# Kernel optimization log

Measured on AMD Instinct MI355X. Metric: run time of the kernel, lower is better.

The kernel has to match this reference:

```python
import jax, jax.numpy as jnp
from jax import lax
import numpy as np

B, CIN, H, W = 8, 3, 512, 512
BASE = 32
TOPK = 200
SCORE_T = 0.01
IOU_T = 0.5
DN = ('NCHW', 'OIHW', 'NCHW')


def setup_inputs() -> dict:
    key = jax.random.key(0)
    ks = jax.random.split(key, 12)
    def conv_w(k, o, i, kh, kw):
        fan_in = i * kh * kw
        return jax.random.normal(k, (o, i, kh, kw), jnp.float32) * (1.0 / np.sqrt(fan_in))
    c = [CIN, BASE, BASE * 2, BASE * 4, BASE * 8]
    inp = {'images': jax.random.normal(ks[0], (B, CIN, H, W), jnp.float32)}
    for l in range(4):
        inp[f'w{l+1}'] = conv_w(ks[1 + 2 * l], c[l + 1], c[l], 3, 3)
        inp[f'b{l+1}'] = jnp.zeros((c[l + 1],), jnp.float32)
    inp['wh'] = conv_w(ks[9], 5, c[4], 1, 1)
    inp['bh'] = jnp.zeros((5,), jnp.float32)
    return inp


def _conv_relu_pool(x, w, b):
    x = lax.conv_general_dilated(x, w, (1, 1), 'SAME', dimension_numbers=DN)
    x = jax.nn.relu(x + b[None, :, None, None])
    return lax.reduce_window(x, -jnp.inf, lax.max, (1, 1, 2, 2), (1, 1, 2, 2), 'VALID')


def _decode(pred):
    # pred: [B,5,Gh,Gw]
    Bn, _, Gh, Gw = pred.shape
    sy, sx = H / float(Gh), W / float(Gw)
    obj = jax.nn.sigmoid(pred[:, 0])
    tx = jax.nn.sigmoid(pred[:, 1])
    ty = jax.nn.sigmoid(pred[:, 2])
    bw = jnp.exp(pred[:, 3]) * sx
    bh = jnp.exp(pred[:, 4]) * sy
    gy = jnp.arange(Gh, dtype=pred.dtype)[None, :, None]
    gx = jnp.arange(Gw, dtype=pred.dtype)[None, None, :]
    cx = gx * sx + tx * sx
    cy = gy * sy + ty * sy
    x1 = jnp.clip(cx - bw / 2.0, 0.0, W - 1)
    y1 = jnp.clip(cy - bh / 2.0, 0.0, H - 1)
    x2 = jnp.clip(cx + bw / 2.0, 0.0, W - 1)
    y2 = jnp.clip(cy + bh / 2.0, 0.0, H - 1)
    boxes = jnp.stack([x1, y1, x2, y2], axis=-1).reshape(Bn, Gh * Gw, 4)
    scores = obj.reshape(Bn, Gh * Gw)
    # score threshold + top-k (fixed size, padded with invalid entries)
    masked = jnp.where(scores >= SCORE_T, scores, -1.0)
    svals, sidx = lax.top_k(masked, TOPK)                      # [B,K]
    boxes_k = jnp.take_along_axis(boxes, sidx[:, :, None], axis=1)  # [B,K,4]
    valid = svals >= SCORE_T
    # pairwise IoU [B,K,K]
    bx1, by1, bx2, by2 = (boxes_k[..., i] for i in range(4))
    area = (bx2 - bx1) * (by2 - by1)
    xx1 = jnp.maximum(bx1[:, :, None], bx1[:, None, :])
    yy1 = jnp.maximum(by1[:, :, None], by1[:, None, :])
    xx2 = jnp.minimum(bx2[:, :, None], bx2[:, None, :])
    yy2 = jnp.minimum(by2[:, :, None], by2[:, None, :])
    inter = jnp.clip(xx2 - xx1, 0.0) * jnp.clip(yy2 - yy1, 0.0)
    union = area[:, :, None] + area[:, None, :] - inter
    iou = inter / jnp.maximum(union, 1e-6)
    ar = jnp.arange(TOPK)
    def body(i, keep):  # greedy NMS over score-sorted boxes
        sup = (iou[:, i, :] > IOU_T) & (ar[None, :] > i) & keep[:, i][:, None]
        return keep & ~sup
    keep = lax.fori_loop(0, TOPK, body, valid)
    scores_k = jnp.where(valid, svals, 0.0)
    return boxes_k, scores_k, keep


def reference(images, w1, b1, w2, b2, w3, b3, w4, b4, wh, bh):
    x = _conv_relu_pool(images, w1, b1)
    x = _conv_relu_pool(x, w2, b2)
    x = _conv_relu_pool(x, w3, b3)
    x = _conv_relu_pool(x, w4, b4)
    pred = lax.conv_general_dilated(x, wh, (1, 1), 'SAME', dimension_numbers=DN)
    pred = pred + bh[None, :, None, None]
    boxes, scores, keep = _decode(pred)
    kf = keep.astype(boxes.dtype)
    out5 = jnp.concatenate([boxes, scores[..., None]], axis=-1) * kf[..., None]
    return out5, keep
```

## Files before the change

### kernel.cpp

```cpp
#include <hip/hip_runtime.h>
#include <math.h>


constexpr int TOPK_N = 200;

template <int CIN, int CI_BLK, int CO_BLK>
__launch_bounds__(256)
__global__ void conv_relu_pool_tiled(const float* __restrict__ in,
                                     const float* __restrict__ wgt,
                                     const float* __restrict__ bias,
                                     float* __restrict__ out,
                                     int Hin, int Win, int Cout) {
    constexpr int SPATIAL = 34 * 34;
    constexpr int SSLOT = (SPATIAL + 255) / 256;
    const int Hp = Hin >> 1, Wp = Win >> 1;
    const int coChunks = Cout / CO_BLK;
    const int b  = blockIdx.z / coChunks;
    const int cz = blockIdx.z % coChunks;
    const int tid = threadIdx.x;
    const int tx = tid & 15, ty = tid >> 4;
    const int px = (blockIdx.x << 4) + tx;
    const int py = (blockIdx.y << 4) + ty;
    const int iy0 = (blockIdx.y << 5) - 1;
    const int ix0 = (blockIdx.x << 5) - 1;

    __shared__ float  s_in[CI_BLK][34][34];
    __shared__ double s_w[CI_BLK * 9 * CO_BLK];
    float* s_in_flat = &s_in[0][0][0];

    int soff[SSLOT];
#pragma unroll
    for (int s = 0; s < SSLOT; ++s) {
        const int cell = tid + s * 256;
        int g = -1;
        if (cell < SPATIAL) {
            const int ly = cell / 34, lx = cell - ly * 34;
            const int iy = iy0 + ly, ix = ix0 + lx;
            if ((unsigned)iy < (unsigned)Hin && (unsigned)ix < (unsigned)Win)
                g = iy * Win + ix;
        }
        soff[s] = g;
    }
    const size_t HW = (size_t)Hin * Win;
    const float* in_b = in + (size_t)b * CIN * HW;

    double acc[CO_BLK][4];
#pragma unroll
    for (int co = 0; co < CO_BLK; ++co)
#pragma unroll
        for (int p = 0; p < 4; ++p) acc[co][p] = 0.0;

    for (int c0 = 0; c0 < CIN; c0 += CI_BLK) {
#pragma unroll
        for (int ci = 0; ci < CI_BLK; ++ci) {
            const float* src = in_b + (c0 + ci) * HW;
#pragma unroll
            for (int s = 0; s < SSLOT; ++s) {
                const int cell = tid + s * 256;
                if (cell < SPATIAL) {
                    const int g = soff[s];
                    float v = 0.f;
                    if (g >= 0) v = src[g];
                    s_in_flat[ci * SPATIAL + cell] = v;
                }
            }
        }
        for (int idx = tid; idx < CI_BLK * 9 * CO_BLK; idx += 256) {
            int co   = idx & (CO_BLK - 1);
            int rest = idx / CO_BLK;
            int k    = rest % 9;
            int ci   = rest / 9;
            s_w[idx] = (double)wgt[((cz * CO_BLK + co) * CIN + c0 + ci) * 9 + k];
        }
        __syncthreads();

#pragma unroll 1
        for (int ci = 0; ci < CI_BLK; ++ci) {
            double win[4][4];
#pragma unroll
            for (int iy = 0; iy < 4; ++iy) {
                float2 r0 = *(const float2*)&s_in[ci][2 * ty + iy][2 * tx];
                float2 r1 = *(const float2*)&s_in[ci][2 * ty + iy][2 * tx + 2];
                win[iy][0] = (double)r0.x; win[iy][1] = (double)r0.y;
                win[iy][2] = (double)r1.x; win[iy][3] = (double)r1.y;
            }
#pragma unroll
            for (int k = 0; k < 9; ++k) {
                const int ky = k / 3, kx = k % 3;
                const double* wp = &s_w[(ci * 9 + k) * CO_BLK];
                double w[CO_BLK];
#pragma unroll
                for (int co = 0; co < CO_BLK; ++co) w[co] = wp[co];
#pragma unroll
                for (int p = 0; p < 4; ++p) {
                    const double v = win[(p >> 1) + ky][(p & 1) + kx];
#pragma unroll
                    for (int co = 0; co < CO_BLK; ++co)
                        acc[co][p] = fma(v, w[co], acc[co][p]);
                }
            }
        }
        __syncthreads();
    }

#pragma unroll
    for (int co = 0; co < CO_BLK; ++co) {
        const double bd = (double)bias[cz * CO_BLK + co];
        const float e0 = fmaxf((float)(acc[co][0] + bd), 0.f);
        const float e1 = fmaxf((float)(acc[co][1] + bd), 0.f);
        const float e2 = fmaxf((float)(acc[co][2] + bd), 0.f);
        const float e3 = fmaxf((float)(acc[co][3] + bd), 0.f);
        out[((size_t)(b * Cout + cz * CO_BLK + co) * Hp + py) * Wp + px] =
            fmaxf(fmaxf(e0, e1), fmaxf(e2, e3));
    }
}

__launch_bounds__(256)
__global__ void head_decode_k(const float* __restrict__ x4,
                              const float* __restrict__ wh,
                              const float* __restrict__ bh,
                              float* __restrict__ boxes,
                              float* __restrict__ scores) {
    __shared__ float s_wh[5 * 256];
    const int tid = threadIdx.x;
#pragma unroll
    for (int i = 0; i < 5; ++i) s_wh[i * 256 + tid] = wh[i * 256 + tid];
    __syncthreads();

    const int idx  = blockIdx.x * 256 + tid;
    const int b    = idx >> 10;
    const int cell = idx & 1023;
    const int gy = cell >> 5, gx = cell & 31;

    double a0 = (double)bh[0], a1 = (double)bh[1], a2 = (double)bh[2],
           a3 = (double)bh[3], a4 = (double)bh[4];
    const float* xp = x4 + b * 262144 + cell;
    for (int ci = 0; ci < 256; ++ci) {
        const double v = (double)xp[ci << 10];
        a0 = fma(v, (double)s_wh[0 * 256 + ci], a0);
        a1 = fma(v, (double)s_wh[1 * 256 + ci], a1);
        a2 = fma(v, (double)s_wh[2 * 256 + ci], a2);
        a3 = fma(v, (double)s_wh[3 * 256 + ci], a3);
        a4 = fma(v, (double)s_wh[4 * 256 + ci], a4);
    }
    const double obj = 1.0 / (1.0 + exp(-a0));
    const double txs = 1.0 / (1.0 + exp(-a1));
    const double tys = 1.0 / (1.0 + exp(-a2));
    const double bw  = exp(a3) * 16.0;
    const double bhh = exp(a4) * 16.0;
    const double cx  = gx * 16.0 + txs * 16.0;
    const double cy  = gy * 16.0 + tys * 16.0;
    float* bp = boxes + idx * 4;
    bp[0] = (float)fmin(fmax(cx - bw * 0.5, 0.0), 511.0);
    bp[1] = (float)fmin(fmax(cy - bhh * 0.5, 0.0), 511.0);
    bp[2] = (float)fmin(fmax(cx + bw * 0.5, 0.0), 511.0);
    bp[3] = (float)fmin(fmax(cy + bhh * 0.5, 0.0), 511.0);
    scores[idx] = (float)obj;
}

__launch_bounds__(256)
__global__ void topk_nms_k(const float* __restrict__ boxes,
                           const float* __restrict__ scores,
                           float* __restrict__ out5,
                           float* __restrict__ keep_out) {
    const int b = blockIdx.x, tid = threadIdx.x;
    __shared__ unsigned long long key[1024];
    __shared__ float bx1[TOPK_N], by1[TOPK_N], bx2[TOPK_N], by2[TOPK_N];
    __shared__ float sv[TOPK_N], ar[TOPK_N];
    __shared__ int   kp[TOPK_N];

    for (int i = tid; i < 1024; i += 256) {
        float s = scores[b * 1024 + i];
        float m = (s >= 0.01f) ? s : -1.0f;
        unsigned u = __float_as_uint(m);
        u = (u & 0x80000000u) ? ~u : (u | 0x80000000u);
        key[i] = ((unsigned long long)u << 32) | (unsigned)(1023 - i);
    }
    __syncthreads();

    for (int k = 2; k <= 1024; k <<= 1) {
        for (int j = k >> 1; j > 0; j >>= 1) {
            for (int i = tid; i < 1024; i += 256) {
                int l = i ^ j;
                if (l > i) {
                    unsigned long long a = key[i], c = key[l];
                    bool desc = ((i & k) == 0);
                    bool sw = desc ? (a < c) : (a > c);
                    if (sw) { key[i] = c; key[l] = a; }
                }
            }
            __syncthreads();
        }
    }

    for (int i = tid; i < TOPK_N; i += 256) {
        unsigned long long kk = key[i];
        unsigned u = (unsigned)(kk >> 32);
        unsigned bits = (u & 0x80000000u) ? (u & 0x7FFFFFFFu) : ~u;
        float s = __uint_as_float(bits);
        int src = 1023 - (int)(kk & 0xFFFFFFFFu);
        const float4 bb = *(const float4*)(boxes + (b * 1024 + src) * 4);
        bx1[i] = bb.x; by1[i] = bb.y; bx2[i] = bb.z; by2[i] = bb.w;
        sv[i] = s;
        ar[i] = (bb.z - bb.x) * (bb.w - bb.y);
        kp[i] = (s >= 0.01f) ? 1 : 0;
    }
    __syncthreads();

    for (int i = 0; i < TOPK_N; ++i) {
        if (kp[i]) {
            const float X1 = bx1[i], Y1 = by1[i], X2 = bx2[i], Y2 = by2[i], A = ar[i];
            for (int j = tid; j < TOPK_N; j += 256) {
                if (j > i && kp[j]) {
                    float xx1 = fmaxf(X1, bx1[j]);
                    float yy1 = fmaxf(Y1, by1[j]);
                    float xx2 = fminf(X2, bx2[j]);
                    float yy2 = fminf(Y2, by2[j]);
                    float inter = fmaxf(xx2 - xx1, 0.f) * fmaxf(yy2 - yy1, 0.f);
                    float uni = A + ar[j] - inter;
                    float iou = inter / fmaxf(uni, 1e-6f);
                    if (iou > 0.5f) kp[j] = 0;
                }
            }
        }
        __syncthreads();
    }

    for (int i = tid; i < TOPK_N; i += 256) {
        float kf = kp[i] ? 1.f : 0.f;
        float s  = sv[i];
        float sc = (s >= 0.01f) ? s : 0.f;
        float* op = out5 + (b * TOPK_N + i) * 5;
        op[0] = bx1[i] * kf;
        op[1] = by1[i] * kf;
        op[2] = bx2[i] * kf;
        op[3] = by2[i] * kf;
        op[4] = sc * kf;
        keep_out[b * TOPK_N + i] = kf;
    }
}

extern "C" void kernel_launch(void* const* d_in, const int* in_sizes, int n_in,
                              void* d_out, int out_size, void* d_ws, size_t ws_size,
                              hipStream_t stream) {
    const float* images = (const float*)d_in[0];
    const float* w1 = (const float*)d_in[1];
    const float* b1 = (const float*)d_in[2];
    const float* w2 = (const float*)d_in[3];
    const float* b2 = (const float*)d_in[4];
    const float* w3 = (const float*)d_in[5];
    const float* b3 = (const float*)d_in[6];
    const float* w4 = (const float*)d_in[7];
    const float* b4 = (const float*)d_in[8];
    const float* wh = (const float*)d_in[9];
    const float* bh = (const float*)d_in[10];
    float* out = (float*)d_out;

    float* A    = (float*)d_ws;
    float* Bbuf = A + 16777216;
    float* boxes  = A + 8388608;
    float* scores = A + 8388608 + 32768;

    conv_relu_pool_tiled<3, 3, 8><<<dim3(16, 16, 8 * 4), 256, 0, stream>>>(
        images, w1, b1, A, 512, 512, 32);
    conv_relu_pool_tiled<32, 2, 8><<<dim3(8, 8, 8 * 8), 256, 0, stream>>>(
        A, w2, b2, Bbuf, 256, 256, 64);
    conv_relu_pool_tiled<64, 2, 8><<<dim3(4, 4, 8 * 16), 256, 0, stream>>>(
        Bbuf, w3, b3, A, 128, 128, 128);
    conv_relu_pool_tiled<128, 2, 8><<<dim3(2, 2, 8 * 32), 256, 0, stream>>>(
        A, w4, b4, Bbuf, 64, 64, 256);
    head_decode_k<<<32, 256, 0, stream>>>(Bbuf, wh, bh, boxes, scores);
    topk_nms_k<<<8, 256, 0, stream>>>(boxes, scores, out, out + 8 * TOPK_N * 5);
}
```

Before: 1.500 ms.

## Double-buffer input and weight tiles in conv-relu-pool kernels via register prefetch

The conv-relu-pool kernel now keeps two shared-memory buffers for the input halo tile and the weights. While the current channel chunk is being computed, the loads for the next chunk are issued into registers, then written to the other buffer with a single barrier per chunk. The goal is to hide global-load latency behind the fp64 FMA work and to remove one of the two barriers per iteration. In exchange it doubles shared-memory use and adds register pressure from the prefetch registers, which may lower occupancy. The weight prefetch assumes NW is at most 256 (one weight per thread), which holds for the current configurations.

Measured after the change: 1.341 ms. 10.6% less time.

```diff
diff --git a/kernel.cpp b/kernel.cpp
--- a/kernel.cpp
+++ b/kernel.cpp
@@ -6,13 +6,15 @@
 
 template <int CIN, int CI_BLK, int CO_BLK>
 __launch_bounds__(256)
-__global__ void conv_relu_pool_tiled(const float* __restrict__ in,
-                                     const float* __restrict__ wgt,
-                                     const float* __restrict__ bias,
-                                     float* __restrict__ out,
-                                     int Hin, int Win, int Cout) {
+__global__ void conv_relu_pool_pipe(const float* __restrict__ in,
+                                    const float* __restrict__ wgt,
+                                    const float* __restrict__ bias,
+                                    float* __restrict__ out,
+                                    int Hin, int Win, int Cout) {
     constexpr int SPATIAL = 34 * 34;
     constexpr int SSLOT = (SPATIAL + 255) / 256;
+    constexpr int NW = CI_BLK * 9 * CO_BLK;
+    constexpr int NCHUNK = CIN / CI_BLK;
     const int Hp = Hin >> 1, Wp = Win >> 1;
     const int coChunks = Cout / CO_BLK;
     const int b  = blockIdx.z / coChunks;
@@ -24,9 +26,8 @@
     const int iy0 = (blockIdx.y << 5) - 1;
     const int ix0 = (blockIdx.x << 5) - 1;
 
-    __shared__ float  s_in[CI_BLK][34][34];
-    __shared__ double s_w[CI_BLK * 9 * CO_BLK];
-    float* s_in_flat = &s_in[0][0][0];
+    __shared__ float  s_in[2][CI_BLK * SPATIAL];
+    __shared__ double s_w[2][NW];
 
     int soff[SSLOT];
 #pragma unroll
@@ -41,6 +42,14 @@
         }
         soff[s] = g;
     }
+    int wg = -1;
+    if (tid < NW) {
+        const int co   = tid & (CO_BLK - 1);
+        const int rest = tid / CO_BLK;
+        const int k    = rest % 9;
+        const int ci   = rest / 9;
+        wg = ((cz * CO_BLK + co) * CIN + ci) * 9 + k;
+    }
     const size_t HW = (size_t)Hin * Win;
     const float* in_b = in + (size_t)b * CIN * HW;
 
@@ -50,44 +59,63 @@
 #pragma unroll
         for (int p = 0; p < 4; ++p) acc[co][p] = 0.0;
 
-    for (int c0 = 0; c0 < CIN; c0 += CI_BLK) {
-#pragma unroll
-        for (int ci = 0; ci < CI_BLK; ++ci) {
-            const float* src = in_b + (c0 + ci) * HW;
-#pragma unroll
-            for (int s = 0; s < SSLOT; ++s) {
-                const int cell = tid + s * 256;
-                if (cell < SPATIAL) {
-                    const int g = soff[s];
+    float rin[CI_BLK][SSLOT];
+    float rw = 0.f;
+
+#pragma unroll
+    for (int ci = 0; ci < CI_BLK; ++ci) {
+        const float* src = in_b + ci * HW;
+#pragma unroll
+        for (int s = 0; s < SSLOT; ++s) {
+            const int cell = tid + s * 256;
+            float v = 0.f;
+            if (cell < SPATIAL) { const int g = soff[s]; if (g >= 0) v = src[g]; }
+            rin[ci][s] = v;
+        }
+    }
+    if (tid < NW) rw = wgt[wg];
+#pragma unroll
+    for (int ci = 0; ci < CI_BLK; ++ci)
+#pragma unroll
+        for (int s = 0; s < SSLOT; ++s) {
+            const int cell = tid + s * 256;
+            if (cell < SPATIAL) s_in[0][ci * SPATIAL + cell] = rin[ci][s];
+        }
+    if (tid < NW) s_w[0][tid] = (double)rw;
+    __syncthreads();
+
+    for (int c = 0; c < NCHUNK; ++c) {
+        const int buf = c & 1;
+        if (c + 1 < NCHUNK) {
+            const int c0n = (c + 1) * CI_BLK;
+#pragma unroll
+            for (int ci = 0; ci < CI_BLK; ++ci) {
+                const float* src = in_b + (c0n + ci) * HW;
+#pragma unroll
+                for (int s = 0; s < SSLOT; ++s) {
+                    const int cell = tid + s * 256;
                     float v = 0.f;
-                    if (g >= 0) v = src[g];
-                    s_in_flat[ci * SPATIAL + cell] = v;
-                }
-            }
-        }
-        for (int idx = tid; idx < CI_BLK * 9 * CO_BLK; idx += 256) {
-            int co   = idx & (CO_BLK - 1);
-            int rest = idx / CO_BLK;
-            int k    = rest % 9;
-            int ci   = rest / 9;
-            s_w[idx] = (double)wgt[((cz * CO_BLK + co) * CIN + c0 + ci) * 9 + k];
-        }
-        __syncthreads();
-
+                    if (cell < SPATIAL) { const int g = soff[s]; if (g >= 0) v = src[g]; }
+                    rin[ci][s] = v;
+                }
+            }
+            if (tid < NW) rw = wgt[wg + c0n * 9];
+        }
 #pragma unroll 1
         for (int ci = 0; ci < CI_BLK; ++ci) {
+            const float* tile = &s_in[buf][ci * SPATIAL];
             double win[4][4];
 #pragma unroll
             for (int iy = 0; iy < 4; ++iy) {
-                float2 r0 = *(const float2*)&s_in[ci][2 * ty + iy][2 * tx];
-                float2 r1 = *(const float2*)&s_in[ci][2 * ty + iy][2 * tx + 2];
+                float2 r0 = *(const float2*)&tile[(2 * ty + iy) * 34 + 2 * tx];
+                float2 r1 = *(const float2*)&tile[(2 * ty + iy) * 34 + 2 * tx + 2];
                 win[iy][0] = (double)r0.x; win[iy][1] = (double)r0.y;
                 win[iy][2] = (double)r1.x; win[iy][3] = (double)r1.y;
             }
 #pragma unroll
             for (int k = 0; k < 9; ++k) {
                 const int ky = k / 3, kx = k % 3;
-                const double* wp = &s_w[(ci * 9 + k) * CO_BLK];
+                const double* wp = &s_w[buf][(ci * 9 + k) * CO_BLK];
                 double w[CO_BLK];
 #pragma unroll
                 for (int co = 0; co < CO_BLK; ++co) w[co] = wp[co];
@@ -100,7 +128,17 @@
                 }
             }
         }
-        __syncthreads();
+        if (c + 1 < NCHUNK) {
+#pragma unroll
+            for (int ci = 0; ci < CI_BLK; ++ci)
+#pragma unroll
+                for (int s = 0; s < SSLOT; ++s) {
+                    const int cell = tid + s * 256;
+                    if (cell < SPATIAL) s_in[buf ^ 1][ci * SPATIAL + cell] = rin[ci][s];
+                }
+            if (tid < NW) s_w[buf ^ 1][tid] = (double)rw;
+            __syncthreads();
+        }
     }
 
 #pragma unroll
@@ -261,13 +299,13 @@
     float* boxes  = A + 8388608;
     float* scores = A + 8388608 + 32768;
 
-    conv_relu_pool_tiled<3, 3, 8><<<dim3(16, 16, 8 * 4), 256, 0, stream>>>(
+    conv_relu_pool_pipe<3, 3, 8><<<dim3(16, 16, 8 * 4), 256, 0, stream>>>(
         images, w1, b1, A, 512, 512, 32);
-    conv_relu_pool_tiled<32, 2, 8><<<dim3(8, 8, 8 * 8), 256, 0, stream>>>(
+    conv_relu_pool_pipe<32, 2, 8><<<dim3(8, 8, 8 * 8), 256, 0, stream>>>(
         A, w2, b2, Bbuf, 256, 256, 64);
-    conv_relu_pool_tiled<64, 2, 8><<<dim3(4, 4, 8 * 16), 256, 0, stream>>>(
+    conv_relu_pool_pipe<64, 2, 8><<<dim3(4, 4, 8 * 16), 256, 0, stream>>>(
         Bbuf, w3, b3, A, 128, 128, 128);
-    conv_relu_pool_tiled<128, 2, 8><<<dim3(2, 2, 8 * 32), 256, 0, stream>>>(
+    conv_relu_pool_pipe<128, 2, 8><<<dim3(2, 2, 8 * 32), 256, 0, stream>>>(
         A, w4, b4, Bbuf, 64, 64, 256);
     head_decode_k<<<32, 256, 0, stream>>>(Bbuf, wh, bh, boxes, scores);
     topk_nms_k<<<8, 256, 0, stream>>>(boxes, scores, out, out + 8 * TOPK_N * 5);
```

## Load conv input windows directly from global memory with register prefetch

Applied to the files above, without the earlier changes.

Drops the shared-memory input tile in the conv+relu+pool kernel. Each thread now loads its own 4x4 input window straight from global memory into registers and prefetches the next channel's window while computing the current one. Weights are still staged in shared memory, now in larger channel chunks so fewer barriers are needed. The cost is redundant global loads, since neighbouring threads re-read overlapping pixels, plus extra register pressure, in exchange for removing the tile staging and its synchronisation.

New measurement: 1.516 ms. About the same (+1.1%).

```diff
diff --git a/kernel.cpp b/kernel.cpp
--- a/kernel.cpp
+++ b/kernel.cpp
@@ -4,15 +4,14 @@
 
 constexpr int TOPK_N = 200;
 
-template <int CIN, int CI_BLK, int CO_BLK>
+template <int CIN, int CI_CHUNK, int CO_BLK>
 __launch_bounds__(256)
-__global__ void conv_relu_pool_tiled(const float* __restrict__ in,
-                                     const float* __restrict__ wgt,
-                                     const float* __restrict__ bias,
-                                     float* __restrict__ out,
-                                     int Hin, int Win, int Cout) {
-    constexpr int SPATIAL = 34 * 34;
-    constexpr int SSLOT = (SPATIAL + 255) / 256;
+__global__ void conv_direct(const float* __restrict__ in,
+                            const float* __restrict__ wgt,
+                            const float* __restrict__ bias,
+                            float* __restrict__ out,
+                            int Hin, int Win, int Cout) {
+    constexpr int NW = CI_CHUNK * 9 * CO_BLK;
     const int Hp = Hin >> 1, Wp = Win >> 1;
     const int coChunks = Cout / CO_BLK;
     const int b  = blockIdx.z / coChunks;
@@ -21,25 +20,21 @@
     const int tx = tid & 15, ty = tid >> 4;
     const int px = (blockIdx.x << 4) + tx;
     const int py = (blockIdx.y << 4) + ty;
-    const int iy0 = (blockIdx.y << 5) - 1;
-    const int ix0 = (blockIdx.x << 5) - 1;
-
-    __shared__ float  s_in[CI_BLK][34][34];
-    __shared__ double s_w[CI_BLK * 9 * CO_BLK];
-    float* s_in_flat = &s_in[0][0][0];
-
-    int soff[SSLOT];
-#pragma unroll
-    for (int s = 0; s < SSLOT; ++s) {
-        const int cell = tid + s * 256;
-        int g = -1;
-        if (cell < SPATIAL) {
-            const int ly = cell / 34, lx = cell - ly * 34;
-            const int iy = iy0 + ly, ix = ix0 + lx;
-            if ((unsigned)iy < (unsigned)Hin && (unsigned)ix < (unsigned)Win)
-                g = iy * Win + ix;
-        }
-        soff[s] = g;
+    const int y0 = 2 * py, x0 = 2 * px;
+
+    __shared__ double s_w[NW];
+
+    int rowE[4], colE[4];
+    float rowM[4], colM[4];
+#pragma unroll
+    for (int d = 0; d < 4; ++d) {
+        int iy = y0 - 1 + d;
+        rowM[d] = (iy >= 0 && iy < Hin) ? 1.f : 0.f;
+        iy = min(max(iy, 0), Hin - 1);
+        rowE[d] = iy * Win;
+        int ix = x0 - 1 + d;
+        colM[d] = (ix >= 0 && ix < Win) ? 1.f : 0.f;
+        colE[d] = min(max(ix, 0), Win - 1);
     }
     const size_t HW = (size_t)Hin * Win;
     const float* in_b = in + (size_t)b * CIN * HW;
@@ -50,44 +45,48 @@
 #pragma unroll
         for (int p = 0; p < 4; ++p) acc[co][p] = 0.0;
 
-    for (int c0 = 0; c0 < CIN; c0 += CI_BLK) {
-#pragma unroll
-        for (int ci = 0; ci < CI_BLK; ++ci) {
-            const float* src = in_b + (c0 + ci) * HW;
-#pragma unroll
-            for (int s = 0; s < SSLOT; ++s) {
-                const int cell = tid + s * 256;
-                if (cell < SPATIAL) {
-                    const int g = soff[s];
-                    float v = 0.f;
-                    if (g >= 0) v = src[g];
-                    s_in_flat[ci * SPATIAL + cell] = v;
-                }
-            }
-        }
-        for (int idx = tid; idx < CI_BLK * 9 * CO_BLK; idx += 256) {
-            int co   = idx & (CO_BLK - 1);
-            int rest = idx / CO_BLK;
-            int k    = rest % 9;
-            int ci   = rest / 9;
-            s_w[idx] = (double)wgt[((cz * CO_BLK + co) * CIN + c0 + ci) * 9 + k];
-        }
+    float raw[16];
+    {
+        const float* src = in_b;
+#pragma unroll
+        for (int dy = 0; dy < 4; ++dy)
+#pragma unroll
+            for (int dx = 0; dx < 4; ++dx)
+                raw[dy * 4 + dx] = src[rowE[dy] + colE[dx]];
+    }
+
+    for (int c0 = 0; c0 < CIN; c0 += CI_CHUNK) {
         __syncthreads();
+        for (int idx = tid; idx < NW; idx += 256) {
+            const int co   = idx & (CO_BLK - 1);
+            const int rest = idx / CO_BLK;
+            const int k    = rest % 9;
+            const int ciL  = rest / 9;
+            s_w[idx] = (double)wgt[((cz * CO_BLK + co) * CIN + c0 + ciL) * 9 + k];
+        }
+        __syncthreads();
 
 #pragma unroll 1
-        for (int ci = 0; ci < CI_BLK; ++ci) {
+        for (int ciL = 0; ciL < CI_CHUNK; ++ciL) {
+            const int ci = c0 + ciL;
             double win[4][4];
 #pragma unroll
-            for (int iy = 0; iy < 4; ++iy) {
-                float2 r0 = *(const float2*)&s_in[ci][2 * ty + iy][2 * tx];
-                float2 r1 = *(const float2*)&s_in[ci][2 * ty + iy][2 * tx + 2];
-                win[iy][0] = (double)r0.x; win[iy][1] = (double)r0.y;
-                win[iy][2] = (double)r1.x; win[iy][3] = (double)r1.y;
+            for (int dy = 0; dy < 4; ++dy)
+#pragma unroll
+                for (int dx = 0; dx < 4; ++dx)
+                    win[dy][dx] = (double)(raw[dy * 4 + dx] * rowM[dy] * colM[dx]);
+            if (ci + 1 < CIN) {
+                const float* src = in_b + (size_t)(ci + 1) * HW;
+#pragma unroll
+                for (int dy = 0; dy < 4; ++dy)
+#pragma unroll
+                    for (int dx = 0; dx < 4; ++dx)
+                        raw[dy * 4 + dx] = src[rowE[dy] + colE[dx]];
             }
 #pragma unroll
             for (int k = 0; k < 9; ++k) {
                 const int ky = k / 3, kx = k % 3;
-                const double* wp = &s_w[(ci * 9 + k) * CO_BLK];
+                const double* wp = &s_w[(ciL * 9 + k) * CO_BLK];
                 double w[CO_BLK];
 #pragma unroll
                 for (int co = 0; co < CO_BLK; ++co) w[co] = wp[co];
@@ -100,7 +99,6 @@
                 }
             }
         }
-        __syncthreads();
     }
 
 #pragma unroll
@@ -261,13 +259,13 @@
     float* boxes  = A + 8388608;
     float* scores = A + 8388608 + 32768;
 
-    conv_relu_pool_tiled<3, 3, 8><<<dim3(16, 16, 8 * 4), 256, 0, stream>>>(
+    conv_direct<3, 3, 8><<<dim3(16, 16, 8 * 4), 256, 0, stream>>>(
         images, w1, b1, A, 512, 512, 32);
-    conv_relu_pool_tiled<32, 2, 8><<<dim3(8, 8, 8 * 8), 256, 0, stream>>>(
+    conv_direct<32, 16, 8><<<dim3(8, 8, 8 * 8), 256, 0, stream>>>(
         A, w2, b2, Bbuf, 256, 256, 64);
-    conv_relu_pool_tiled<64, 2, 8><<<dim3(4, 4, 8 * 16), 256, 0, stream>>>(
+    conv_direct<64, 16, 8><<<dim3(4, 4, 8 * 16), 256, 0, stream>>>(
         Bbuf, w3, b3, A, 128, 128, 128);
-    conv_relu_pool_tiled<128, 2, 8><<<dim3(2, 2, 8 * 32), 256, 0, stream>>>(
+    conv_direct<128, 16, 8><<<dim3(2, 2, 8 * 32), 256, 0, stream>>>(
         A, w4, b4, Bbuf, 64, 64, 256);
     head_decode_k<<<32, 256, 0, stream>>>(Bbuf, wh, bh, boxes, scores);
     topk_nms_k<<<8, 256, 0, stream>>>(boxes, scores, out, out + 8 * TOPK_N * 5);
```
